# Optimization experiments

Hardware: AMD Instinct MI355X
Metric: run time of the kernel (lower is better)

## Reference

```python
import jax, jax.numpy as jnp
import numpy as np

# dims: batch, input, output, state, heads, shifts, slot size, num addresses
B, IN, OUT, ST, H, NSHIFT, M, N = 256, 256, 256, 512, 4, 3, 64, 1024
READ = H * M
PPH = NSHIFT + 1 + M + M + M + 1 + 1  # per-head params: s, gamma, erase, add, k, beta, g
UPD = H * PPH
D = IN + ST + READ  # controller input width
_IDX = np.cumsum([0, NSHIFT, 1, M, M, M, 1, 1]).tolist()


def setup_inputs() -> dict:
    key = jax.random.key(0)
    ks = jax.random.split(key, 8)
    sc = 0.05
    tm_input = jax.random.normal(ks[0], (B, IN), jnp.float32)
    tm_state = jax.random.uniform(ks[1], (B, ST), jnp.float32)
    wt = jax.nn.softmax(jax.random.normal(ks[2], (B, H, N), jnp.float32), axis=-1)
    mem = jax.random.normal(ks[3], (B, N, M), jnp.float32) * 0.1
    return {
        'tm_input': tm_input, 'tm_state': tm_state, 'wt': wt, 'mem': mem,
        'W_i2w': jax.random.normal(ks[4], (H, ST + IN), jnp.float32) * sc,
        'b_i2w': jnp.zeros((H,), jnp.float32),
        'W_i2s': jax.random.normal(ks[5], (ST, D), jnp.float32) * sc,
        'b_i2s': jnp.zeros((ST,), jnp.float32),
        'W_i2o': jax.random.normal(ks[6], (OUT, D), jnp.float32) * sc,
        'b_i2o': jnp.zeros((OUT,), jnp.float32),
        'W_i2u': jax.random.normal(ks[7], (UPD, D), jnp.float32) * sc,
        'b_i2u': jnp.zeros((UPD,), jnp.float32),
    }


def _ntm_cell(tm_input, tm_state, wt, mem,
              W_i2w, b_i2w, W_i2s, b_i2s, W_i2o, b_i2o, W_i2u, b_i2u):
    # --- gated reset of attention toward address 0 ---
    combined = jnp.concatenate([tm_state, tm_input], axis=-1)        # [B, ST+IN]
    f = jax.nn.sigmoid(combined @ W_i2w.T + b_i2w)[..., None]        # [B, H, 1]
    wt0 = jnp.zeros_like(wt).at[:, :, 0].set(1.0)
    wt = f * wt0 + (1.0 - f) * wt                                    # [B, H, N]

    # --- interface read ---
    read = jnp.einsum('bhn,bnm->bhm', wt, mem).reshape(wt.shape[0], READ)

    # --- controller ---
    c = jnp.concatenate([tm_input, tm_state, read], axis=-1)         # [B, D]
    tm_state_new = jax.nn.sigmoid(c @ W_i2s.T + b_i2s)
    tm_output = jax.nn.sigmoid(c @ W_i2o.T + b_i2o)
    ud = (c @ W_i2u.T + b_i2u).reshape(-1, H, PPH)                   # [B, H, PPH]

    # --- split + activate interface parameters ---
    s_sh  = jax.nn.softmax(jax.nn.softplus(ud[..., _IDX[0]:_IDX[1]]), axis=-1)  # shift
    gamma = 1.0 + jax.nn.softplus(ud[..., _IDX[1]:_IDX[2]])                      # sharpening
    erase = jax.nn.sigmoid(ud[..., _IDX[2]:_IDX[3]])
    add   = jnp.tanh(ud[..., _IDX[3]:_IDX[4]])
    k     = jnp.tanh(ud[..., _IDX[4]:_IDX[5]])
    beta  = jax.nn.softplus(ud[..., _IDX[5]:_IDX[6]])
    g     = jax.nn.sigmoid(ud[..., _IDX[6]:_IDX[7]])

    # --- write: multiplicative erase over heads, then additive write ---
    keep = jnp.prod(1.0 - wt[..., None] * erase[:, :, None, :], axis=1)  # [B, N, M]
    mem = mem * keep + jnp.einsum('bhn,bhm->bnm', wt, add)

    # --- content addressing (cosine similarity) + gated interpolation ---
    kn = k / (jnp.linalg.norm(k, axis=-1, keepdims=True) + 1e-8)
    mn = mem / (jnp.linalg.norm(mem, axis=-1, keepdims=True) + 1e-8)
    sim = jnp.einsum('bhm,bnm->bhn', kn, mn)
    wt = g * jax.nn.softmax(beta * sim, axis=-1) + (1.0 - g) * wt

    # --- circular convolution with the shift kernel ---
    zone = NSHIFT // 2
    wt = sum(s_sh[..., j + zone, None] * jnp.roll(wt, j, axis=-1)
             for j in range(-zone, zone + 1))

    # --- sharpening + L1 renormalization ---
    wt = (wt + 1e-12) ** gamma
    wt = wt / jnp.sum(wt, axis=-1, keepdims=True)

    return tm_output, tm_state_new, wt, mem


def reference(tm_input, tm_state, wt, mem,
              W_i2w, b_i2w, W_i2s, b_i2s, W_i2o, b_i2o, W_i2u, b_i2u):
    return _ntm_cell(tm_input, tm_state, wt, mem,
                     W_i2w, b_i2w, W_i2s, b_i2s, W_i2o, b_i2o, W_i2u, b_i2u)
```

## Files before the change

kernel.cpp:

```cpp
#include <hip/hip_runtime.h>
#include <math.h>

#define B_    256
#define IN_   256
#define OUT_  256
#define ST_   512
#define H_    4
#define M_    64
#define N_    1024
#define D_    1024
#define PPH_  198
#define UPD_  792
#define NTOT  1560
#define CP_   1600
#define KS_   4

typedef unsigned short ushort_;
typedef unsigned int uint_;

typedef __attribute__((ext_vector_type(8))) short bf16x8;
typedef __attribute__((ext_vector_type(4))) float f32x4;

__device__ __forceinline__ float sigmoidf_(float x){ return 1.f/(1.f+__expf(-x)); }
__device__ __forceinline__ float softplusf_(float x){
    float ax = fabsf(x);
    return fmaxf(x, 0.f) + log1pf(__expf(-ax));
}
__device__ __forceinline__ ushort_ f2bf(float f){
    uint_ u = __float_as_uint(f);
    u += 0x7fffu + ((u >> 16) & 1u);
    return (ushort_)(u >> 16);
}

__global__ __launch_bounds__(256) void k_wconv(
    const float* __restrict__ W_i2s, const float* __restrict__ W_i2o,
    const float* __restrict__ W_i2u, ushort_* __restrict__ Wb)
{
    const int idx = (blockIdx.x*256 + threadIdx.x) * 8;
    const float* src;
    if (idx < 512*1024)      src = W_i2s + idx;
    else if (idx < 768*1024) src = W_i2o + (idx - 512*1024);
    else                     src = W_i2u + (idx - 768*1024);
    float4 v0 = *(const float4*)src;
    float4 v1 = *(const float4*)(src + 4);
    union { ushort_ u[8]; uint4 q; } r;
    r.u[0]=f2bf(v0.x); r.u[1]=f2bf(v0.y); r.u[2]=f2bf(v0.z); r.u[3]=f2bf(v0.w);
    r.u[4]=f2bf(v1.x); r.u[5]=f2bf(v1.y); r.u[6]=f2bf(v1.z); r.u[7]=f2bf(v1.w);
    *(uint4*)(Wb + idx) = r.q;
}

__global__ __launch_bounds__(1024) void k_gate_read(
    const float* __restrict__ tm_input, const float* __restrict__ tm_state,
    const float* __restrict__ wt, const float* __restrict__ mem,
    const float* __restrict__ W_i2w, const float* __restrict__ b_i2w,
    float* __restrict__ wt_g, ushort_* __restrict__ cB)
{
    __shared__ float wt_s[N_*H_];
    __shared__ float part[16][H_][M_];
    __shared__ float f_s[H_];
    const int b = blockIdx.x, tid = threadIdx.x;
    const int wave = tid >> 6, lane = tid & 63;

    if (wave < H_) {
        float pa = 0.f;
        const float* Wrow = W_i2w + wave*(ST_+IN_);
        const float* st  = tm_state + (size_t)b*ST_;
        const float* inp = tm_input + (size_t)b*IN_;
        #pragma unroll
        for (int k = 0; k < 12; ++k) {
            int i = lane + 64*k;
            float v = (i < ST_) ? st[i] : inp[i - ST_];
            pa += v * Wrow[i];
        }
        #pragma unroll
        for (int m = 32; m; m >>= 1) pa += __shfl_xor(pa, m, 64);
        if (lane == 0) f_s[wave] = sigmoidf_(pa + b_i2w[wave]);
    }
    if (tid < 256)      cB[(size_t)b*D_ + tid] = f2bf(tm_input[(size_t)b*IN_ + tid]);
    else if (tid < 768) cB[(size_t)b*D_ + tid] = f2bf(tm_state[(size_t)b*ST_ + tid - 256]);
    __syncthreads();

    {
        const int h = tid & 3;
        const int nb = tid >> 2;
        const float f = f_s[h];
        #pragma unroll
        for (int i = 0; i < 4; ++i) {
            const int n = nb + 256*i;
            float v = (1.f - f) * wt[((size_t)b*H_ + h)*N_ + n];
            if (n == 0) v += f;
            wt_s[n*4 + h] = v;
            wt_g[((size_t)b*H_ + h)*N_ + n] = v;
        }
    }
    __syncthreads();

    {
        const int m4 = lane & 15, ro = lane >> 4;
        const float4* mp = (const float4*)(mem + (size_t)b*N_*M_);
        float4 a0 = make_float4(0.f,0.f,0.f,0.f), a1 = a0, a2 = a0, a3 = a0;
        #pragma unroll
        for (int r = 0; r < 16; ++r) {
            const int n = wave*64 + r*4 + ro;
            const float4 mv = mp[n*16 + m4];
            const float4 wv = *(const float4*)&wt_s[n*4];
            a0.x += wv.x*mv.x; a0.y += wv.x*mv.y; a0.z += wv.x*mv.z; a0.w += wv.x*mv.w;
            a1.x += wv.y*mv.x; a1.y += wv.y*mv.y; a1.z += wv.y*mv.z; a1.w += wv.y*mv.w;
            a2.x += wv.z*mv.x; a2.y += wv.z*mv.y; a2.z += wv.z*mv.z; a2.w += wv.z*mv.w;
            a3.x += wv.w*mv.x; a3.y += wv.w*mv.y; a3.z += wv.w*mv.z; a3.w += wv.w*mv.w;
        }
        #pragma unroll
        for (int msk = 16; msk <= 32; msk <<= 1) {
            a0.x += __shfl_xor(a0.x, msk, 64); a0.y += __shfl_xor(a0.y, msk, 64);
            a0.z += __shfl_xor(a0.z, msk, 64); a0.w += __shfl_xor(a0.w, msk, 64);
            a1.x += __shfl_xor(a1.x, msk, 64); a1.y += __shfl_xor(a1.y, msk, 64);
            a1.z += __shfl_xor(a1.z, msk, 64); a1.w += __shfl_xor(a1.w, msk, 64);
            a2.x += __shfl_xor(a2.x, msk, 64); a2.y += __shfl_xor(a2.y, msk, 64);
            a2.z += __shfl_xor(a2.z, msk, 64); a2.w += __shfl_xor(a2.w, msk, 64);
            a3.x += __shfl_xor(a3.x, msk, 64); a3.y += __shfl_xor(a3.y, msk, 64);
            a3.z += __shfl_xor(a3.z, msk, 64); a3.w += __shfl_xor(a3.w, msk, 64);
        }
        if (ro == 0) {
            *(float4*)&part[wave][0][m4*4] = a0;
            *(float4*)&part[wave][1][m4*4] = a1;
            *(float4*)&part[wave][2][m4*4] = a2;
            *(float4*)&part[wave][3][m4*4] = a3;
        }
    }
    __syncthreads();
    if (tid < 256) {
        const int hh = tid >> 6, m = tid & 63;
        float r = 0.f;
        #pragma unroll
        for (int w = 0; w < 16; ++w) r += part[w][hh][m];
        cB[(size_t)b*D_ + IN_ + ST_ + tid] = f2bf(r);
    }
}

__global__ __launch_bounds__(256) void k_ctrl_gemm_mfma(
    const ushort_* __restrict__ cB, const ushort_* __restrict__ Wb,
    float* __restrict__ P)
{
    const int tid = threadIdx.x;
    const int w = tid >> 6, lane = tid & 63;
    const int wr = w >> 1, wc = w & 1;
    const int b0 = blockIdx.y * 64 + wr * 32;
    const int o0 = blockIdx.x * 64 + wc * 32;
    const int kb = blockIdx.z * (D_ / KS_);
    const int lrow = lane & 15, lk = (lane >> 4) * 8;

    const bf16x8* a0p = (const bf16x8*)(cB + (size_t)(b0 + lrow)*D_ + kb + lk);
    const bf16x8* a1p = (const bf16x8*)(cB + (size_t)(b0 + 16 + lrow)*D_ + kb + lk);
    const int oc0 = min(o0 + lrow, NTOT-1);
    const int oc1 = min(o0 + 16 + lrow, NTOT-1);
    const bf16x8* b0p = (const bf16x8*)(Wb + (size_t)oc0*D_ + kb + lk);
    const bf16x8* b1p = (const bf16x8*)(Wb + (size_t)oc1*D_ + kb + lk);

    f32x4 acc00 = {0.f,0.f,0.f,0.f}, acc01 = acc00, acc10 = acc00, acc11 = acc00;
    #pragma unroll
    for (int ks = 0; ks < (D_/KS_)/32; ++ks) {
        bf16x8 av0 = a0p[ks*4];
        bf16x8 av1 = a1p[ks*4];
        bf16x8 bv0 = b0p[ks*4];
        bf16x8 bv1 = b1p[ks*4];
        acc00 = __builtin_amdgcn_mfma_f32_16x16x32_bf16(av0, bv0, acc00, 0, 0, 0);
        acc01 = __builtin_amdgcn_mfma_f32_16x16x32_bf16(av0, bv1, acc01, 0, 0, 0);
        acc10 = __builtin_amdgcn_mfma_f32_16x16x32_bf16(av1, bv0, acc10, 0, 0, 0);
        acc11 = __builtin_amdgcn_mfma_f32_16x16x32_bf16(av1, bv1, acc11, 0, 0, 0);
    }

    float* Pp = P + (size_t)blockIdx.z * (B_*CP_);
    const int rsub = (lane >> 4) * 4;
    #pragma unroll
    for (int mi = 0; mi < 2; ++mi) {
        #pragma unroll
        for (int ni = 0; ni < 2; ++ni) {
            f32x4 v = (mi == 0) ? (ni == 0 ? acc00 : acc01)
                                : (ni == 0 ? acc10 : acc11);
            const int o = o0 + ni*16 + lrow;
            const int rbase = b0 + mi*16 + rsub;
            #pragma unroll
            for (int r = 0; r < 4; ++r)
                Pp[(size_t)(rbase + r)*CP_ + o] = v[r];
        }
    }
}

__global__ __launch_bounds__(256) void k_merge(
    const float* __restrict__ P,
    const float* __restrict__ b_i2s, const float* __restrict__ b_i2o,
    const float* __restrict__ b_i2u,
    float* __restrict__ out, float* __restrict__ ud)
{
    const int o = blockIdx.x*256 + threadIdx.x;
    if (o >= NTOT) return;
    const int b = blockIdx.y;
    const size_t base = (size_t)b*CP_ + o;
    float v = P[base] + P[(size_t)B_*CP_ + base]
            + P[(size_t)2*B_*CP_ + base] + P[(size_t)3*B_*CP_ + base];
    if (o < ST_) {
        out[(size_t)B_*OUT_ + (size_t)b*ST_ + o] = sigmoidf_(v + b_i2s[o]);
    } else if (o < ST_ + OUT_) {
        const int oo = o - ST_;
        out[(size_t)b*OUT_ + oo] = sigmoidf_(v + b_i2o[oo]);
    } else {
        const int oo = o - ST_ - OUT_;
        ud[(size_t)b*UPD_ + oo] = v + b_i2u[oo];
    }
}

__global__ __launch_bounds__(64) void k_params(
    const float* __restrict__ ud,
    float* __restrict__ erase, float* __restrict__ addv,
    float* __restrict__ kn, float* __restrict__ sc)
{
    const int bh = blockIdx.x;
    const int m = threadIdx.x;
    const float* u = ud + (size_t)(bh >> 2)*UPD_ + (bh & 3)*PPH_;

    float e  = sigmoidf_(u[4 + m]);
    float a  = tanhf(u[68 + m]);
    float kv = tanhf(u[132 + m]);
    float s2 = kv*kv;
    #pragma unroll
    for (int msk = 32; msk; msk >>= 1) s2 += __shfl_xor(s2, msk, 64);
    float knv = kv / (sqrtf(s2) + 1e-8f);

    erase[bh*M_ + m] = e;
    addv [bh*M_ + m] = a;
    kn   [bh*M_ + m] = knv;

    if (m == 0) {
        float p0 = softplusf_(u[0]), p1 = softplusf_(u[1]), p2 = softplusf_(u[2]);
        float mx = fmaxf(p0, fmaxf(p1, p2));
        float e0 = __expf(p0-mx), e1 = __expf(p1-mx), e2 = __expf(p2-mx);
        float inv = 1.f/(e0+e1+e2);
        sc[bh*6+0] = e0*inv; sc[bh*6+1] = e1*inv; sc[bh*6+2] = e2*inv;
        sc[bh*6+3] = 1.f + softplusf_(u[3]);
        sc[bh*6+4] = softplusf_(u[196]);
        sc[bh*6+5] = sigmoidf_(u[197]);
    }
}

__global__ __launch_bounds__(256) void k_mem_sim(
    const float* __restrict__ mem, const float* __restrict__ wt_g,
    const float* __restrict__ erase, const float* __restrict__ addv,
    const float* __restrict__ kn,
    float* __restrict__ mem_out, float* __restrict__ sim)
{
    __shared__ float es[H_*M_], as[H_*M_], ks[H_*M_];
    const int tid = threadIdx.x;
    const int b = blockIdx.x >> 4;
    const int chunk = blockIdx.x & 15;
    const int wave = tid >> 6, lane = tid & 63;
    const int q = lane & 3, rloc = lane >> 2;
    const int n = chunk*64 + wave*16 + rloc;

    es[tid] = erase[(b << 8) + tid];
    as[tid] = addv [(b << 8) + tid];
    ks[tid] = kn   [(b << 8) + tid];
    __syncthreads();

    const float w0 = wt_g[((size_t)b*H_ + 0)*N_ + n];
    const float w1 = wt_g[((size_t)b*H_ + 1)*N_ + n];
    const float w2 = wt_g[((size_t)b*H_ + 2)*N_ + n];
    const float w3 = wt_g[((size_t)b*H_ + 3)*N_ + n];

    const float4* mp = (const float4*)(mem     + ((size_t)b*N_ + n)*M_ + q*16);
    float4*       op = (float4*)      (mem_out + ((size_t)b*N_ + n)*M_ + q*16);

    float nrm = 0.f, p0 = 0.f, p1 = 0.f, p2 = 0.f, p3 = 0.f;
    #pragma unroll
    for (int jj = 0; jj < 4; ++jj) {
        const int c4 = q*16 + jj*4;
        const float4 o  = mp[jj];
        const float4 e0 = *(const float4*)&es[      c4];
        const float4 e1 = *(const float4*)&es[ 64 + c4];
        const float4 e2 = *(const float4*)&es[128 + c4];
        const float4 e3 = *(const float4*)&es[192 + c4];
        const float4 a0 = *(const float4*)&as[      c4];
        const float4 a1 = *(const float4*)&as[ 64 + c4];
        const float4 a2 = *(const float4*)&as[128 + c4];
        const float4 a3 = *(const float4*)&as[192 + c4];
        const float4 k0 = *(const float4*)&ks[      c4];
        const float4 k1 = *(const float4*)&ks[ 64 + c4];
        const float4 k2 = *(const float4*)&ks[128 + c4];
        const float4 k3 = *(const float4*)&ks[192 + c4];

        float4 nm;
        nm.x = o.x*((1.f-w0*e0.x)*(1.f-w1*e1.x)*(1.f-w2*e2.x)*(1.f-w3*e3.x))
             + (w0*a0.x + w1*a1.x + w2*a2.x + w3*a3.x);
        nm.y = o.y*((1.f-w0*e0.y)*(1.f-w1*e1.y)*(1.f-w2*e2.y)*(1.f-w3*e3.y))
             + (w0*a0.y + w1*a1.y + w2*a2.y + w3*a3.y);
        nm.z = o.z*((1.f-w0*e0.z)*(1.f-w1*e1.z)*(1.f-w2*e2.z)*(1.f-w3*e3.z))
             + (w0*a0.z + w1*a1.z + w2*a2.z + w3*a3.z);
        nm.w = o.w*((1.f-w0*e0.w)*(1.f-w1*e1.w)*(1.f-w2*e2.w)*(1.f-w3*e3.w))
             + (w0*a0.w + w1*a1.w + w2*a2.w + w3*a3.w);
        op[jj] = nm;

        nrm += nm.x*nm.x + nm.y*nm.y + nm.z*nm.z + nm.w*nm.w;
        p0 += k0.x*nm.x + k0.y*nm.y + k0.z*nm.z + k0.w*nm.w;
        p1 += k1.x*nm.x + k1.y*nm.y + k1.z*nm.z + k1.w*nm.w;
        p2 += k2.x*nm.x + k2.y*nm.y + k2.z*nm.z + k2.w*nm.w;
        p3 += k3.x*nm.x + k3.y*nm.y + k3.z*nm.z + k3.w*nm.w;
    }
    #pragma unroll
    for (int msk = 1; msk <= 2; msk <<= 1) {
        nrm += __shfl_xor(nrm, msk, 64);
        p0  += __shfl_xor(p0,  msk, 64);
        p1  += __shfl_xor(p1,  msk, 64);
        p2  += __shfl_xor(p2,  msk, 64);
        p3  += __shfl_xor(p3,  msk, 64);
    }
    const float inv = 1.f/(sqrtf(nrm) + 1e-8f);
    const float pv = (q == 0) ? p0 : (q == 1) ? p1 : (q == 2) ? p2 : p3;
    sim[((size_t)b*H_ + q)*N_ + n] = pv*inv;
}

__global__ __launch_bounds__(256) void k_wt_final(
    const float* __restrict__ sim, const float* __restrict__ wt_g,
    const float* __restrict__ sc, float* __restrict__ wt_out)
{
    __shared__ float wc[N_];
    __shared__ float red[8];
    const int bh = blockIdx.x, tid = threadIdx.x, wave = tid >> 6, lane = tid & 63;
    const float* sp = sc + bh*6;
    const float s0 = sp[0], s1 = sp[1], s2 = sp[2], gamma = sp[3], beta = sp[4], g = sp[5];
    const float* simp = sim + (size_t)bh*N_;
    const float* wgp  = wt_g + (size_t)bh*N_;

    float x[4];
    float mx = -1e30f;
    #pragma unroll
    for (int i = 0; i < 4; ++i) { x[i] = beta*simp[tid + 256*i]; mx = fmaxf(mx, x[i]); }
    #pragma unroll
    for (int msk = 32; msk; msk >>= 1) mx = fmaxf(mx, __shfl_xor(mx, msk, 64));
    if (lane == 0) red[wave] = mx;
    __syncthreads();
    mx = fmaxf(fmaxf(red[0], red[1]), fmaxf(red[2], red[3]));

    float e[4]; float sum = 0.f;
    #pragma unroll
    for (int i = 0; i < 4; ++i) { e[i] = __expf(x[i] - mx); sum += e[i]; }
    #pragma unroll
    for (int msk = 32; msk; msk >>= 1) sum += __shfl_xor(sum, msk, 64);
    if (lane == 0) red[4 + wave] = sum;
    __syncthreads();
    sum = red[4] + red[5] + red[6] + red[7];
    const float inv = 1.f/sum;

    #pragma unroll
    for (int i = 0; i < 4; ++i) {
        int n = tid + 256*i;
        wc[n] = g*e[i]*inv + (1.f - g)*wgp[n];
    }
    __syncthreads();

    float y[4]; float ysum = 0.f;
    #pragma unroll
    for (int i = 0; i < 4; ++i) {
        int n = tid + 256*i;
        float v = s0*wc[(n+1) & (N_-1)] + s1*wc[n] + s2*wc[(n-1) & (N_-1)];
        y[i] = __powf(v + 1e-12f, gamma);
        ysum += y[i];
    }
    #pragma unroll
    for (int msk = 32; msk; msk >>= 1) ysum += __shfl_xor(ysum, msk, 64);
    __syncthreads();
    if (lane == 0) red[wave] = ysum;
    __syncthreads();
    ysum = red[0] + red[1] + red[2] + red[3];
    const float yinv = 1.f/ysum;
    #pragma unroll
    for (int i = 0; i < 4; ++i)
        wt_out[(size_t)bh*N_ + tid + 256*i] = y[i]*yinv;
}

extern "C" void kernel_launch(void* const* d_in, const int* in_sizes, int n_in,
                              void* d_out, int out_size, void* d_ws, size_t ws_size,
                              hipStream_t stream)
{
    const float* tm_input = (const float*)d_in[0];
    const float* tm_state = (const float*)d_in[1];
    const float* wt       = (const float*)d_in[2];
    const float* mem      = (const float*)d_in[3];
    const float* W_i2w    = (const float*)d_in[4];
    const float* b_i2w    = (const float*)d_in[5];
    const float* W_i2s    = (const float*)d_in[6];
    const float* b_i2s    = (const float*)d_in[7];
    const float* W_i2o    = (const float*)d_in[8];
    const float* b_i2o    = (const float*)d_in[9];
    const float* W_i2u    = (const float*)d_in[10];
    const float* b_i2u    = (const float*)d_in[11];

    float* out = (float*)d_out;
    float* ws  = (float*)d_ws;

    float*   wt_g  = ws;
    ushort_* cB    = (ushort_*)(ws + 1048576);
    float*   ud    = ws + 1179648;
    float*   erase = ws + 1382400;
    float*   addv  = ws + 1447936;
    float*   kn    = ws + 1513472;
    float*   sc    = ws + 1579008;
    ushort_* Wb    = (ushort_*)(ws + 1585152);
    float*   P     = ws + 2383872;

    float* out_wt  = out + 196608;
    float* out_mem = out + 1245184;

    hipLaunchKernelGGL(k_wconv, dim3(780), dim3(256), 0, stream,
                       W_i2s, W_i2o, W_i2u, Wb);
    hipLaunchKernelGGL(k_gate_read, dim3(B_), dim3(1024), 0, stream,
                       tm_input, tm_state, wt, mem, W_i2w, b_i2w, wt_g, cB);
    hipLaunchKernelGGL(k_ctrl_gemm_mfma, dim3(25, 4, KS_), dim3(256), 0, stream,
                       cB, Wb, P);
    hipLaunchKernelGGL(k_merge, dim3(7, B_), dim3(256), 0, stream,
                       P, b_i2s, b_i2o, b_i2u, out, ud);
    hipLaunchKernelGGL(k_params, dim3(B_*H_), dim3(64), 0, stream,
                       ud, erase, addv, kn, sc);
    hipLaunchKernelGGL(k_mem_sim, dim3(B_*16), dim3(256), 0, stream,
                       mem, wt_g, erase, addv, kn, out_mem, out_wt);
    hipLaunchKernelGGL(k_wt_final, dim3(B_*H_), dim3(256), 0, stream,
                       out_wt, wt_g, sc, out_wt);
}
```

Measured before the change: 84.75 us.

## Split gate/read kernel into gate, chunked partial read, and merge kernels

Replaces the single 1024-thread per-batch gate+read kernel with three kernels. A 256-thread gate kernel, a read kernel gridded over 8 address chunks per batch that writes partial sums to workspace, and a merge kernel that reduces the chunks into the bf16 controller input. The aim is more parallelism and occupancy for the memory-bound read of mem, which was limited to 256 large blocks. In exchange it adds two kernel launches, writes wt_g to global memory and reads it back, and adds a partial-sum round trip.

```diff
diff --git a/kernel.cpp b/kernel.cpp
--- a/kernel.cpp
+++ b/kernel.cpp
@@ -14,6 +14,7 @@
 #define NTOT  1560
 #define CP_   1600
 #define KS_   4
+#define RCH_  8
 
 typedef unsigned short ushort_;
 typedef unsigned int uint_;
@@ -49,23 +50,21 @@
     *(uint4*)(Wb + idx) = r.q;
 }
 
-__global__ __launch_bounds__(1024) void k_gate_read(
+__global__ __launch_bounds__(256) void k_gate(
     const float* __restrict__ tm_input, const float* __restrict__ tm_state,
-    const float* __restrict__ wt, const float* __restrict__ mem,
+    const float* __restrict__ wt,
     const float* __restrict__ W_i2w, const float* __restrict__ b_i2w,
     float* __restrict__ wt_g, ushort_* __restrict__ cB)
 {
-    __shared__ float wt_s[N_*H_];
-    __shared__ float part[16][H_][M_];
     __shared__ float f_s[H_];
     const int b = blockIdx.x, tid = threadIdx.x;
     const int wave = tid >> 6, lane = tid & 63;
-
-    if (wave < H_) {
+    const float* st  = tm_state + (size_t)b*ST_;
+    const float* inp = tm_input + (size_t)b*IN_;
+
+    {
         float pa = 0.f;
         const float* Wrow = W_i2w + wave*(ST_+IN_);
-        const float* st  = tm_state + (size_t)b*ST_;
-        const float* inp = tm_input + (size_t)b*IN_;
         #pragma unroll
         for (int k = 0; k < 12; ++k) {
             int i = lane + 64*k;
@@ -76,65 +75,89 @@
         for (int m = 32; m; m >>= 1) pa += __shfl_xor(pa, m, 64);
         if (lane == 0) f_s[wave] = sigmoidf_(pa + b_i2w[wave]);
     }
-    if (tid < 256)      cB[(size_t)b*D_ + tid] = f2bf(tm_input[(size_t)b*IN_ + tid]);
-    else if (tid < 768) cB[(size_t)b*D_ + tid] = f2bf(tm_state[(size_t)b*ST_ + tid - 256]);
-    __syncthreads();
-
+    #pragma unroll
+    for (int i = 0; i < 3; ++i) {
+        int j = tid + 256*i;
+        cB[(size_t)b*D_ + j] = f2bf(j < IN_ ? inp[j] : st[j - IN_]);
+    }
+    __syncthreads();
+
+    #pragma unroll
+    for (int i = 0; i < 16; ++i) {
+        int idx = tid + 256*i;
+        int h = idx >> 10, n = idx & (N_-1);
+        float f = f_s[h];
+        float v = (1.f - f) * wt[((size_t)b*H_ + h)*N_ + n];
+        if (n == 0) v += f;
+        wt_g[(size_t)b*H_*N_ + idx] = v;
+    }
+}
+
+__global__ __launch_bounds__(256) void k_read_part(
+    const float* __restrict__ mem, const float* __restrict__ wt_g,
+    float* __restrict__ Pr)
+{
+    __shared__ float wt_sl[128*H_];
+    __shared__ float part[4][H_][M_];
+    const int b = blockIdx.y, chunk = blockIdx.x, tid = threadIdx.x;
+    const int wave = tid >> 6, lane = tid & 63;
+    const int m4 = lane & 15, ro = lane >> 4;
+    const int nbase = chunk * 128;
+
+    #pragma unroll
+    for (int i = 0; i < 2; ++i) {
+        int idx = tid + 256*i;
+        int h = idx & 3, nl = idx >> 2;
+        wt_sl[idx] = wt_g[((size_t)b*H_ + h)*N_ + nbase + nl];
+    }
+    __syncthreads();
+
+    const float4* mp = (const float4*)(mem + ((size_t)b*N_ + nbase)*M_);
+    float4 a0 = make_float4(0.f,0.f,0.f,0.f), a1 = a0, a2 = a0, a3 = a0;
+    #pragma unroll
+    for (int r = 0; r < 8; ++r) {
+        const int nl = wave*32 + r*4 + ro;
+        const float4 mv = mp[nl*16 + m4];
+        const float4 wv = *(const float4*)&wt_sl[nl*4];
+        a0.x += wv.x*mv.x; a0.y += wv.x*mv.y; a0.z += wv.x*mv.z; a0.w += wv.x*mv.w;
+        a1.x += wv.y*mv.x; a1.y += wv.y*mv.y; a1.z += wv.y*mv.z; a1.w += wv.y*mv.w;
+        a2.x += wv.z*mv.x; a2.y += wv.z*mv.y; a2.z += wv.z*mv.z; a2.w += wv.z*mv.w;
+        a3.x += wv.w*mv.x; a3.y += wv.w*mv.y; a3.z += wv.w*mv.z; a3.w += wv.w*mv.w;
+    }
+    #pragma unroll
+    for (int msk = 16; msk <= 32; msk <<= 1) {
+        a0.x += __shfl_xor(a0.x, msk, 64); a0.y += __shfl_xor(a0.y, msk, 64);
+        a0.z += __shfl_xor(a0.z, msk, 64); a0.w += __shfl_xor(a0.w, msk, 64);
+        a1.x += __shfl_xor(a1.x, msk, 64); a1.y += __shfl_xor(a1.y, msk, 64);
+        a1.z += __shfl_xor(a1.z, msk, 64); a1.w += __shfl_xor(a1.w, msk, 64);
+        a2.x += __shfl_xor(a2.x, msk, 64); a2.y += __shfl_xor(a2.y, msk, 64);
+        a2.z += __shfl_xor(a2.z, msk, 64); a2.w += __shfl_xor(a2.w, msk, 64);
+        a3.x += __shfl_xor(a3.x, msk, 64); a3.y += __shfl_xor(a3.y, msk, 64);
+        a3.z += __shfl_xor(a3.z, msk, 64); a3.w += __shfl_xor(a3.w, msk, 64);
+    }
+    if (ro == 0) {
+        *(float4*)&part[wave][0][m4*4] = a0;
+        *(float4*)&part[wave][1][m4*4] = a1;
+        *(float4*)&part[wave][2][m4*4] = a2;
+        *(float4*)&part[wave][3][m4*4] = a3;
+    }
+    __syncthreads();
     {
-        const int h = tid & 3;
-        const int nb = tid >> 2;
-        const float f = f_s[h];
-        #pragma unroll
-        for (int i = 0; i < 4; ++i) {
-            const int n = nb + 256*i;
-            float v = (1.f - f) * wt[((size_t)b*H_ + h)*N_ + n];
-            if (n == 0) v += f;
-            wt_s[n*4 + h] = v;
-            wt_g[((size_t)b*H_ + h)*N_ + n] = v;
-        }
-    }
-    __syncthreads();
-
-    {
-        const int m4 = lane & 15, ro = lane >> 4;
-        const float4* mp = (const float4*)(mem + (size_t)b*N_*M_);
-        float4 a0 = make_float4(0.f,0.f,0.f,0.f), a1 = a0, a2 = a0, a3 = a0;
-        #pragma unroll
-        for (int r = 0; r < 16; ++r) {
-            const int n = wave*64 + r*4 + ro;
-            const float4 mv = mp[n*16 + m4];
-            const float4 wv = *(const float4*)&wt_s[n*4];
-            a0.x += wv.x*mv.x; a0.y += wv.x*mv.y; a0.z += wv.x*mv.z; a0.w += wv.x*mv.w;
-            a1.x += wv.y*mv.x; a1.y += wv.y*mv.y; a1.z += wv.y*mv.z; a1.w += wv.y*mv.w;
-            a2.x += wv.z*mv.x; a2.y += wv.z*mv.y; a2.z += wv.z*mv.z; a2.w += wv.z*mv.w;
-            a3.x += wv.w*mv.x; a3.y += wv.w*mv.y; a3.z += wv.w*mv.z; a3.w += wv.w*mv.w;
-        }
-        #pragma unroll
-        for (int msk = 16; msk <= 32; msk <<= 1) {
-            a0.x += __shfl_xor(a0.x, msk, 64); a0.y += __shfl_xor(a0.y, msk, 64);
-            a0.z += __shfl_xor(a0.z, msk, 64); a0.w += __shfl_xor(a0.w, msk, 64);
-            a1.x += __shfl_xor(a1.x, msk, 64); a1.y += __shfl_xor(a1.y, msk, 64);
-            a1.z += __shfl_xor(a1.z, msk, 64); a1.w += __shfl_xor(a1.w, msk, 64);
-            a2.x += __shfl_xor(a2.x, msk, 64); a2.y += __shfl_xor(a2.y, msk, 64);
-            a2.z += __shfl_xor(a2.z, msk, 64); a2.w += __shfl_xor(a2.w, msk, 64);
-            a3.x += __shfl_xor(a3.x, msk, 64); a3.y += __shfl_xor(a3.y, msk, 64);
-            a3.z += __shfl_xor(a3.z, msk, 64); a3.w += __shfl_xor(a3.w, msk, 64);
-        }
-        if (ro == 0) {
-            *(float4*)&part[wave][0][m4*4] = a0;
-            *(float4*)&part[wave][1][m4*4] = a1;
-            *(float4*)&part[wave][2][m4*4] = a2;
-            *(float4*)&part[wave][3][m4*4] = a3;
-        }
-    }
-    __syncthreads();
-    if (tid < 256) {
-        const int hh = tid >> 6, m = tid & 63;
-        float r = 0.f;
-        #pragma unroll
-        for (int w = 0; w < 16; ++w) r += part[w][hh][m];
-        cB[(size_t)b*D_ + IN_ + ST_ + tid] = f2bf(r);
-    }
+        const int h = tid >> 6, m = tid & 63;
+        float r = part[0][h][m] + part[1][h][m] + part[2][h][m] + part[3][h][m];
+        Pr[((size_t)(b*RCH_ + chunk))*256 + tid] = r;
+    }
+}
+
+__global__ __launch_bounds__(256) void k_read_merge(
+    const float* __restrict__ Pr, ushort_* __restrict__ cB)
+{
+    const int b = blockIdx.x, tid = threadIdx.x;
+    float r = 0.f;
+    #pragma unroll
+    for (int c = 0; c < RCH_; ++c)
+        r += Pr[((size_t)(b*RCH_ + c))*256 + tid];
+    cB[(size_t)b*D_ + IN_ + ST_ + tid] = f2bf(r);
 }
 
 __global__ __launch_bounds__(256) void k_ctrl_gemm_mfma(
@@ -405,14 +428,19 @@
     float*   sc    = ws + 1579008;
     ushort_* Wb    = (ushort_*)(ws + 1585152);
     float*   P     = ws + 2383872;
+    float*   Pr    = ws + 4022272;
 
     float* out_wt  = out + 196608;
     float* out_mem = out + 1245184;
 
     hipLaunchKernelGGL(k_wconv, dim3(780), dim3(256), 0, stream,
                        W_i2s, W_i2o, W_i2u, Wb);
-    hipLaunchKernelGGL(k_gate_read, dim3(B_), dim3(1024), 0, stream,
-                       tm_input, tm_state, wt, mem, W_i2w, b_i2w, wt_g, cB);
+    hipLaunchKernelGGL(k_gate, dim3(B_), dim3(256), 0, stream,
+                       tm_input, tm_state, wt, W_i2w, b_i2w, wt_g, cB);
+    hipLaunchKernelGGL(k_read_part, dim3(RCH_, B_), dim3(256), 0, stream,
+                       mem, wt_g, Pr);
+    hipLaunchKernelGGL(k_read_merge, dim3(B_), dim3(256), 0, stream,
+                       Pr, cB);
     hipLaunchKernelGGL(k_ctrl_gemm_mfma, dim3(25, 4, KS_), dim3(256), 0, stream,
                        cB, Wb, P);
     hipLaunchKernelGGL(k_merge, dim3(7, B_), dim3(256), 0, stream,
```

Result: slower. 87.84 us (+3.6%).
